# Performance work log

Measured on AMD Instinct MI355X. Metric: run time of the kernel, lower is better.

The kernel has to match this reference:

```python
import jax, jax.numpy as jnp
import numpy as np

NEG = -1e30  # log-space 'zero' (avoids -inf NaN issues under jit)
EPS = 1e-7   # keras.backend.epsilon()


def _ctc_loss(y_true, y_pred):
    # y_true: [B, L] int labels in [0, C-1), y_pred: [B, T, C] softmax probs.
    # Keras ctc_batch_cost: logits = log(y_pred + eps), then tf.nn.ctc_loss
    # (which applies log_softmax internally), blank = C - 1.
    B, T, C = y_pred.shape
    L = y_true.shape[1]
    S = 2 * L + 1
    blank = C - 1

    logp = jax.nn.log_softmax(jnp.log(y_pred + EPS), axis=-1)  # [B, T, C]

    # Extended label sequence: blank, l1, blank, l2, ..., blank  -> [B, S]
    ext = jnp.full((B, S), blank, dtype=y_true.dtype).at[:, 1::2].set(y_true)
    lp_ext = jnp.take_along_axis(logp, ext[:, None, :].astype(jnp.int32), axis=2)  # [B, T, S]

    # skip transition s-2 -> s allowed iff ext[s] != blank and ext[s] != ext[s-2]
    ext_m2 = jnp.concatenate([jnp.full((B, 2), blank, ext.dtype), ext[:, :-2]], axis=1)
    allow_skip = (ext != blank) & (ext != ext_m2)
    allow_skip = allow_skip.at[:, :2].set(False)

    # alpha init at t=0
    alpha = jnp.full((B, S), NEG, dtype=logp.dtype)
    alpha = alpha.at[:, 0].set(lp_ext[:, 0, 0]).at[:, 1].set(lp_ext[:, 0, 1])

    neg1 = jnp.full((B, 1), NEG, dtype=logp.dtype)
    neg2 = jnp.full((B, 2), NEG, dtype=logp.dtype)

    def step(a, lp_t):
        prev1 = jnp.concatenate([neg1, a[:, :-1]], axis=1)
        prev2 = jnp.concatenate([neg2, a[:, :-2]], axis=1)
        acc = jnp.logaddexp(a, prev1)
        acc = jnp.where(allow_skip, jnp.logaddexp(acc, prev2), acc)
        return acc + lp_t, None

    lp_seq = jnp.transpose(lp_ext, (1, 0, 2))[1:]  # [T-1, B, S]
    alpha, _ = jax.lax.scan(step, alpha, lp_seq)

    loss = -jnp.logaddexp(alpha[:, -1], alpha[:, -2])  # [B]
    return loss[:, None]  # [B, 1] like keras ctc_batch_cost


def setup_inputs() -> dict:
    key = jax.random.key(0)
    k1, k2 = jax.random.split(key)
    B, T, C, L = 1024, 256, 128, 64
    y_true = jax.random.randint(k1, (B, L), 0, C - 1, dtype=jnp.int32)
    y_pred = jax.random.uniform(k2, (B, T, C), dtype=jnp.float32, minval=1e-4, maxval=1.0)
    return {"y_true": y_true, "y_pred": y_pred}


def reference(y_true, y_pred):
    return _ctc_loss(y_true, y_pred)
```

## Files before the change

kernel.cpp:

```cpp
#include <hip/hip_runtime.h>
#include <math.h>

#define BATCH 1024
#define TT    256
#define CC    128
#define LL    64
#define EPSV  (1e-7f)

typedef float f32x4 __attribute__((ext_vector_type(4)));

template <int CTRL>
__device__ __forceinline__ float dpp0(float x) {
    return __int_as_float(__builtin_amdgcn_update_dpp(0, __float_as_int(x), CTRL, 0xF, 0xF, true));
}
template <int CTRL>
__device__ __forceinline__ float dppS(float x) {
    return __int_as_float(__builtin_amdgcn_update_dpp(__float_as_int(x), __float_as_int(x), CTRL, 0xF, 0xF, false));
}
__device__ __forceinline__ float rol1_f(float x) {
    return __int_as_float(__builtin_amdgcn_update_dpp(__float_as_int(x), __float_as_int(x), 0x134, 0xF, 0xF, false));
}
__device__ __forceinline__ int rol1_i(int x) {
    return __builtin_amdgcn_update_dpp(x, x, 0x134, 0xF, 0xF, false);
}
__device__ __forceinline__ float rdlane(float x, int l) {
    return __int_as_float(__builtin_amdgcn_readlane(__float_as_int(x), l));
}
__device__ __forceinline__ float wave_max_bcast(float m) {
    m = fmaxf(m, dppS<0x111>(m));
    m = fmaxf(m, dppS<0x112>(m));
    m = fmaxf(m, dppS<0x114>(m));
    m = fmaxf(m, dppS<0x118>(m));
    m = fmaxf(m, dppS<0x142>(m));
    m = fmaxf(m, dppS<0x143>(m));
    return rdlane(m, 63);
}
__device__ __forceinline__ unsigned f2h(float x) {
    _Float16 h = (_Float16)x;
    unsigned short u; __builtin_memcpy(&u, &h, 2);
    return (unsigned)u;
}
__device__ __forceinline__ float h2f(unsigned short u) {
    _Float16 h; __builtin_memcpy(&h, &u, 2);
    return (float)h;
}

__global__ __launch_bounds__(512, 8) void ctc_fwd_kernel(const int* __restrict__ y_true,
                                                         const float* __restrict__ y_pred,
                                                         float* __restrict__ out) {
    __shared__ unsigned short qtab[TT][66];
    __shared__ float qblank[TT];
    __shared__ float logZpart[8];

    const int b    = blockIdx.x;
    const int tid  = threadIdx.x;
    const int wv   = tid >> 6;
    const int lane = tid & 63;

    const float* yp = y_pred + (size_t)b * (TT * CC);
    const int lab  = y_true[b * LL + lane];
    const int srcA = lab >> 2;
    const int srcB = 32 + srcA;
    const bool hiPair = (lab & 2) != 0;
    const bool hiHalf = (lab & 1) != 0;

    const int off = ((lane >> 5) << 7) + ((lane & 31) << 2);
    const float* base = yp + off;

    float zacc = 0.0f;
    f32x4 v[4];
    #pragma unroll
    for (int j = 0; j < 4; ++j)
        v[j] = __builtin_nontemporal_load((const f32x4*)(base + 256 * (wv + 8 * j)));

    for (int g = 0; g < 4; ++g) {
        f32x4 vn[4];
        if (g < 3) {
            #pragma unroll
            for (int j = 0; j < 4; ++j)
                vn[j] = __builtin_nontemporal_load((const f32x4*)(base + 256 * (wv + 32 * (g + 1) + 8 * j)));
        }
        #pragma unroll
        for (int j = 0; j < 4; ++j) {
            const int r2 = wv + 32 * g + 8 * j;
            const int tA = 2 * r2, tB = tA + 1;
            float q0 = v[j][0] + EPSV, q1 = v[j][1] + EPSV;
            float q2 = v[j][2] + EPSV, q3 = v[j][3] + EPSV;
            float s = (q0 + q1) + (q2 + q3);
            s += dpp0<0x111>(s);
            s += dpp0<0x112>(s);
            s += dpp0<0x114>(s);
            s += dpp0<0x118>(s);
            s += dpp0<0x142>(s);
            zacc += __logf(s);
            int i01 = (int)(f2h(q0) | (f2h(q1) << 16));
            int i23 = (int)(f2h(q2) | (f2h(q3) << 16));
            int gA01 = __shfl(i01, srcA), gA23 = __shfl(i23, srcA);
            int gB01 = __shfl(i01, srcB), gB23 = __shfl(i23, srcB);
            int sA = hiPair ? gA23 : gA01;
            int sB = hiPair ? gB23 : gB01;
            qtab[tA][lane] = (unsigned short)(hiHalf ? ((unsigned)sA >> 16) : (sA & 0xFFFF));
            qtab[tB][lane] = (unsigned short)(hiHalf ? ((unsigned)sB >> 16) : (sB & 0xFFFF));
            if ((lane & 31) == 31) qblank[tA + (lane >> 5)] = q3;
        }
        #pragma unroll
        for (int j = 0; j < 4; ++j) v[j] = vn[j];
    }
    {
        float z31 = rdlane(zacc, 31), z63 = rdlane(zacc, 63);
        if (lane == 0) logZpart[wv] = z31 + z63;
    }
    __syncthreads();

    if (wv == 0) {
        float logZ = 0.0f;
        #pragma unroll
        for (int w = 0; w < 8; ++w) logZ += logZpart[w];

        const int labm1  = rol1_i(lab);
        const float mskip = (lane >= 1 && lab != labm1) ? 1.0f : 0.0f;
        const bool l0 = (lane == 0);

        float a0 = l0 ? qblank[0] : 0.0f;
        float a1 = l0 ? h2f(qtab[0][lane]) : 0.0f;
        float aX = 0.0f;
        int Esum = 0;

        float qbv[8], qlv[8];
        #pragma unroll
        for (int i = 0; i < 8; ++i) {
            qbv[i] = qblank[1 + i];
            qlv[i] = h2f(qtab[1 + i][lane]);
        }

        for (int t0 = 1; t0 + 8 <= TT; t0 += 8) {
            float qbn[8], qln[8];
            #pragma unroll
            for (int i = 0; i < 8; ++i) {
                int tn = t0 + 8 + i; tn = (tn < TT) ? tn : (TT - 1);
                qbn[i] = qblank[tn];
                qln[i] = h2f(qtab[tn][lane]);
            }
            #pragma unroll
            for (int i = 0; i < 8; ++i) {
                float nb  = rol1_f(a1);
                float na0 = (a0 + (l0 ? 0.0f : nb)) * qbv[i];
                float na1 = fmaf(mskip, nb, a0 + a1) * qlv[i];
                aX = l0 ? (aX + nb) * qbv[i] : 0.0f;
                a0 = na0; a1 = na1;
            }
            float m = fmaxf(fmaxf(a0, a1), aX);
            float mall = wave_max_bcast(m);
            int ex = (int)((__float_as_uint(mall) >> 23) & 0xFF);
            int e  = 127 - ex;
            float sc = __uint_as_float((unsigned)(127 + e) << 23);
            a0 *= sc; a1 *= sc; aX *= sc;
            Esum += e;
            #pragma unroll
            for (int i = 0; i < 8; ++i) { qbv[i] = qbn[i]; qlv[i] = qln[i]; }
        }
        #pragma unroll
        for (int i = 0; i < 7; ++i) {
            float nb  = rol1_f(a1);
            float na0 = (a0 + (l0 ? 0.0f : nb)) * qbv[i];
            float na1 = fmaf(mskip, nb, a0 + a1) * qlv[i];
            aX = l0 ? (aX + nb) * qbv[i] : 0.0f;
            a0 = na0; a1 = na1;
        }
        float a127 = rdlane(a1, 63);
        if (lane == 0) {
            float tot = aX + a127;
            out[b] = logZ + (float)Esum * 0.69314718055994531f - __logf(tot);
        }
    }
}

extern "C" void kernel_launch(void* const* d_in, const int* in_sizes, int n_in,
                              void* d_out, int out_size, void* d_ws, size_t ws_size,
                              hipStream_t stream) {
    const int*   y_true = (const int*)d_in[0];
    const float* y_pred = (const float*)d_in[1];
    float*       out    = (float*)d_out;
    ctc_fwd_kernel<<<BATCH, 512, 0, stream>>>(y_true, y_pred, out);
}
```

Before: 37.38 us.

## Interleave CTC alpha recursion with staged probability loading per time chunk

Splits the time axis into four stages with a block barrier after each. Wave 0 runs the alpha recursion on the finished chunk while the other waves load and convert the next chunk, so the serial scan no longer waits for the whole table to be built. Loads switch from nontemporal to ordinary, and the next chunk's prefetch now comes after the current chunk is processed. The trade-off is three extra barriers, raised priority for wave 0, and possible stalls when the scan stage takes longer than the load stage.

```diff
diff --git a/kernel.cpp b/kernel.cpp
--- a/kernel.cpp
+++ b/kernel.cpp
@@ -67,19 +67,20 @@
     const int off = ((lane >> 5) << 7) + ((lane & 31) << 2);
     const float* base = yp + off;
 
+    const int   labm1 = rol1_i(lab);
+    const float mskip = (lane >= 1 && lab != labm1) ? 1.0f : 0.0f;
+    const bool  l0 = (lane == 0);
+    float a0 = 0.0f, a1 = 0.0f, aX = 0.0f;
+    int   Esum = 0;
     float zacc = 0.0f;
+
     f32x4 v[4];
     #pragma unroll
     for (int j = 0; j < 4; ++j)
-        v[j] = __builtin_nontemporal_load((const f32x4*)(base + 256 * (wv + 8 * j)));
+        v[j] = *(const f32x4*)(base + 256 * (wv + 8 * j));
 
+    #pragma unroll
     for (int g = 0; g < 4; ++g) {
-        f32x4 vn[4];
-        if (g < 3) {
-            #pragma unroll
-            for (int j = 0; j < 4; ++j)
-                vn[j] = __builtin_nontemporal_load((const f32x4*)(base + 256 * (wv + 32 * (g + 1) + 8 * j)));
-        }
         #pragma unroll
         for (int j = 0; j < 4; ++j) {
             const int r2 = wv + 32 * g + 8 * j;
@@ -103,74 +104,74 @@
             qtab[tB][lane] = (unsigned short)(hiHalf ? ((unsigned)sB >> 16) : (sB & 0xFFFF));
             if ((lane & 31) == 31) qblank[tA + (lane >> 5)] = q3;
         }
-        #pragma unroll
-        for (int j = 0; j < 4; ++j) v[j] = vn[j];
+        if (g < 3) {
+            #pragma unroll
+            for (int j = 0; j < 4; ++j)
+                v[j] = *(const f32x4*)(base + 256 * (wv + 32 * (g + 1) + 8 * j));
+        }
+        if (g == 3) {
+            float z31 = rdlane(zacc, 31), z63 = rdlane(zacc, 63);
+            if (lane == 0) logZpart[wv] = z31 + z63;
+        }
+        asm volatile("s_waitcnt lgkmcnt(0)" ::: "memory");
+        __builtin_amdgcn_s_barrier();
+        __builtin_amdgcn_sched_barrier(0);
+
+        if (wv == 0) {
+            __builtin_amdgcn_s_setprio(1);
+            if (g == 0) {
+                a0 = l0 ? qblank[0] : 0.0f;
+                a1 = l0 ? h2f(qtab[0][lane]) : 0.0f;
+                aX = 0.0f;
+            }
+            const int s0 = (g == 0) ? 1 : (64 * g - 7);
+            const int nc = (g == 0) ? 7 : 8;
+            for (int c = 0; c < nc; ++c) {
+                const int s = s0 + 8 * c;
+                float qb[8], ql[8];
+                #pragma unroll
+                for (int i = 0; i < 8; ++i) {
+                    qb[i] = qblank[s + i];
+                    ql[i] = h2f(qtab[s + i][lane]);
+                }
+                #pragma unroll
+                for (int i = 0; i < 8; ++i) {
+                    float nb  = rol1_f(a1);
+                    float na0 = (a0 + (l0 ? 0.0f : nb)) * qb[i];
+                    float na1 = fmaf(mskip, nb, a0 + a1) * ql[i];
+                    aX = l0 ? (aX + nb) * qb[i] : 0.0f;
+                    a0 = na0; a1 = na1;
+                }
+                float m = fmaxf(fmaxf(a0, a1), aX);
+                float mall = wave_max_bcast(m);
+                int ex = (int)((__float_as_uint(mall) >> 23) & 0xFF);
+                int e  = 127 - ex;
+                float sc = __uint_as_float((unsigned)(127 + e) << 23);
+                a0 *= sc; a1 *= sc; aX *= sc;
+                Esum += e;
+            }
+            __builtin_amdgcn_s_setprio(0);
+        }
     }
-    {
-        float z31 = rdlane(zacc, 31), z63 = rdlane(zacc, 63);
-        if (lane == 0) logZpart[wv] = z31 + z63;
-    }
-    __syncthreads();
 
     if (wv == 0) {
-        float logZ = 0.0f;
-        #pragma unroll
-        for (int w = 0; w < 8; ++w) logZ += logZpart[w];
-
-        const int labm1  = rol1_i(lab);
-        const float mskip = (lane >= 1 && lab != labm1) ? 1.0f : 0.0f;
-        const bool l0 = (lane == 0);
-
-        float a0 = l0 ? qblank[0] : 0.0f;
-        float a1 = l0 ? h2f(qtab[0][lane]) : 0.0f;
-        float aX = 0.0f;
-        int Esum = 0;
-
-        float qbv[8], qlv[8];
-        #pragma unroll
-        for (int i = 0; i < 8; ++i) {
-            qbv[i] = qblank[1 + i];
-            qlv[i] = h2f(qtab[1 + i][lane]);
-        }
-
-        for (int t0 = 1; t0 + 8 <= TT; t0 += 8) {
-            float qbn[8], qln[8];
-            #pragma unroll
-            for (int i = 0; i < 8; ++i) {
-                int tn = t0 + 8 + i; tn = (tn < TT) ? tn : (TT - 1);
-                qbn[i] = qblank[tn];
-                qln[i] = h2f(qtab[tn][lane]);
-            }
-            #pragma unroll
-            for (int i = 0; i < 8; ++i) {
-                float nb  = rol1_f(a1);
-                float na0 = (a0 + (l0 ? 0.0f : nb)) * qbv[i];
-                float na1 = fmaf(mskip, nb, a0 + a1) * qlv[i];
-                aX = l0 ? (aX + nb) * qbv[i] : 0.0f;
-                a0 = na0; a1 = na1;
-            }
-            float m = fmaxf(fmaxf(a0, a1), aX);
-            float mall = wave_max_bcast(m);
-            int ex = (int)((__float_as_uint(mall) >> 23) & 0xFF);
-            int e  = 127 - ex;
-            float sc = __uint_as_float((unsigned)(127 + e) << 23);
-            a0 *= sc; a1 *= sc; aX *= sc;
-            Esum += e;
-            #pragma unroll
-            for (int i = 0; i < 8; ++i) { qbv[i] = qbn[i]; qlv[i] = qln[i]; }
-        }
         #pragma unroll
         for (int i = 0; i < 7; ++i) {
+            float qb = qblank[249 + i];
+            float ql = h2f(qtab[249 + i][lane]);
             float nb  = rol1_f(a1);
-            float na0 = (a0 + (l0 ? 0.0f : nb)) * qbv[i];
-            float na1 = fmaf(mskip, nb, a0 + a1) * qlv[i];
-            aX = l0 ? (aX + nb) * qbv[i] : 0.0f;
+            float na0 = (a0 + (l0 ? 0.0f : nb)) * qb;
+            float na1 = fmaf(mskip, nb, a0 + a1) * ql;
+            aX = l0 ? (aX + nb) * qb : 0.0f;
             a0 = na0; a1 = na1;
         }
+        float LZ = 0.0f;
+        #pragma unroll
+        for (int w = 0; w < 8; ++w) LZ += logZpart[w];
         float a127 = rdlane(a1, 63);
         if (lane == 0) {
             float tot = aX + a127;
-            out[b] = logZ + (float)Esum * 0.69314718055994531f - __logf(tot);
+            out[b] = LZ + (float)Esum * 0.69314718055994531f - __logf(tot);
         }
     }
 }
```

Result: slower. 46.22 us (+23.6%).

## Process four batch items per block, overlapping the DP with the next item's loads

Applied to the files above, without the earlier changes.

Each block now handles four batch items with double-buffered shared tables. Wave 0 runs the serial alpha recursion for the current item at raised priority, while the other seven waves stream and pack the next item's probabilities. This hides the single-wave DP latency behind memory traffic. In exchange there are four times fewer blocks (256), more shared memory per block, plain loads in place of nontemporal ones, and the first item is not overlapped.

```diff
diff --git a/kernel.cpp b/kernel.cpp
--- a/kernel.cpp
+++ b/kernel.cpp
@@ -6,6 +6,8 @@
 #define CC    128
 #define LL    64
 #define EPSV  (1e-7f)
+#define ITEMS 4
+#define NBLK  (BATCH / ITEMS)
 
 typedef float f32x4 __attribute__((ext_vector_type(4)));
 
@@ -45,133 +47,157 @@
     return (float)h;
 }
 
-__global__ __launch_bounds__(512, 8) void ctc_fwd_kernel(const int* __restrict__ y_true,
-                                                         const float* __restrict__ y_pred,
-                                                         float* __restrict__ out) {
-    __shared__ unsigned short qtab[TT][66];
-    __shared__ float qblank[TT];
-    __shared__ float logZpart[8];
-
-    const int b    = blockIdx.x;
-    const int tid  = threadIdx.x;
-    const int wv   = tid >> 6;
-    const int lane = tid & 63;
-
-    const float* yp = y_pred + (size_t)b * (TT * CC);
-    const int lab  = y_true[b * LL + lane];
-    const int srcA = lab >> 2;
-    const int srcB = 32 + srcA;
+template <int NPAIRS, int STRIDE, int DEPTH>
+__device__ __forceinline__ void stream_item(const float* __restrict__ base,
+                                            int start, int lab, int lane,
+                                            unsigned short (* __restrict__ qt)[66],
+                                            float* __restrict__ qb,
+                                            float* __restrict__ lzslot) {
+    const int  srcA   = lab >> 2;
+    const int  srcB   = 32 + srcA;
     const bool hiPair = (lab & 2) != 0;
     const bool hiHalf = (lab & 1) != 0;
 
-    const int off = ((lane >> 5) << 7) + ((lane & 31) << 2);
-    const float* base = yp + off;
-
     float zacc = 0.0f;
-    f32x4 v[4];
-    #pragma unroll
-    for (int j = 0; j < 4; ++j)
-        v[j] = __builtin_nontemporal_load((const f32x4*)(base + 256 * (wv + 8 * j)));
-
-    for (int g = 0; g < 4; ++g) {
-        f32x4 vn[4];
-        if (g < 3) {
-            #pragma unroll
-            for (int j = 0; j < 4; ++j)
-                vn[j] = __builtin_nontemporal_load((const f32x4*)(base + 256 * (wv + 32 * (g + 1) + 8 * j)));
-        }
-        #pragma unroll
-        for (int j = 0; j < 4; ++j) {
-            const int r2 = wv + 32 * g + 8 * j;
-            const int tA = 2 * r2, tB = tA + 1;
-            float q0 = v[j][0] + EPSV, q1 = v[j][1] + EPSV;
-            float q2 = v[j][2] + EPSV, q3 = v[j][3] + EPSV;
-            float s = (q0 + q1) + (q2 + q3);
-            s += dpp0<0x111>(s);
-            s += dpp0<0x112>(s);
-            s += dpp0<0x114>(s);
-            s += dpp0<0x118>(s);
-            s += dpp0<0x142>(s);
-            zacc += __logf(s);
-            int i01 = (int)(f2h(q0) | (f2h(q1) << 16));
-            int i23 = (int)(f2h(q2) | (f2h(q3) << 16));
-            int gA01 = __shfl(i01, srcA), gA23 = __shfl(i23, srcA);
-            int gB01 = __shfl(i01, srcB), gB23 = __shfl(i23, srcB);
-            int sA = hiPair ? gA23 : gA01;
-            int sB = hiPair ? gB23 : gB01;
-            qtab[tA][lane] = (unsigned short)(hiHalf ? ((unsigned)sA >> 16) : (sA & 0xFFFF));
-            qtab[tB][lane] = (unsigned short)(hiHalf ? ((unsigned)sB >> 16) : (sB & 0xFFFF));
-            if ((lane & 31) == 31) qblank[tA + (lane >> 5)] = q3;
-        }
-        #pragma unroll
-        for (int j = 0; j < 4; ++j) v[j] = vn[j];
-    }
-    {
-        float z31 = rdlane(zacc, 31), z63 = rdlane(zacc, 63);
-        if (lane == 0) logZpart[wv] = z31 + z63;
-    }
-    __syncthreads();
-
-    if (wv == 0) {
-        float logZ = 0.0f;
-        #pragma unroll
-        for (int w = 0; w < 8; ++w) logZ += logZpart[w];
-
-        const int labm1  = rol1_i(lab);
-        const float mskip = (lane >= 1 && lab != labm1) ? 1.0f : 0.0f;
-        const bool l0 = (lane == 0);
-
-        float a0 = l0 ? qblank[0] : 0.0f;
-        float a1 = l0 ? h2f(qtab[0][lane]) : 0.0f;
-        float aX = 0.0f;
-        int Esum = 0;
-
-        float qbv[8], qlv[8];
+    f32x4 v[DEPTH];
+    #pragma unroll
+    for (int d = 0; d < DEPTH; ++d) {
+        int r2 = start + STRIDE * d; r2 = (r2 < 128) ? r2 : 127;
+        v[d] = *(const f32x4*)(base + 256 * r2);
+    }
+    #pragma unroll
+    for (int i = 0; i < NPAIRS; ++i) {
+        const int  r2i   = start + STRIDE * i;
+        const bool valid = (r2i < 128);
+        const int  r2    = valid ? r2i : 127;
+        f32x4 x = v[i % DEPTH];
+        if (i + DEPTH < NPAIRS) {
+            int rn = start + STRIDE * (i + DEPTH); rn = (rn < 128) ? rn : 127;
+            v[i % DEPTH] = *(const f32x4*)(base + 256 * rn);
+        }
+        const int tA = 2 * r2, tB = tA + 1;
+        float q0 = x[0] + EPSV, q1 = x[1] + EPSV;
+        float q2 = x[2] + EPSV, q3 = x[3] + EPSV;
+        float s = (q0 + q1) + (q2 + q3);
+        s += dpp0<0x111>(s);
+        s += dpp0<0x112>(s);
+        s += dpp0<0x114>(s);
+        s += dpp0<0x118>(s);
+        s += dpp0<0x142>(s);
+        if (valid) zacc += __logf(s);
+        int i01 = (int)(f2h(q0) | (f2h(q1) << 16));
+        int i23 = (int)(f2h(q2) | (f2h(q3) << 16));
+        int gA01 = __shfl(i01, srcA), gA23 = __shfl(i23, srcA);
+        int gB01 = __shfl(i01, srcB), gB23 = __shfl(i23, srcB);
+        int sA = hiPair ? gA23 : gA01;
+        int sB = hiPair ? gB23 : gB01;
+        qt[tA][lane] = (unsigned short)(hiHalf ? ((unsigned)sA >> 16) : (sA & 0xFFFF));
+        qt[tB][lane] = (unsigned short)(hiHalf ? ((unsigned)sB >> 16) : (sB & 0xFFFF));
+        if ((lane & 31) == 31) qb[tA + (lane >> 5)] = q3;
+    }
+    float z31 = rdlane(zacc, 31), z63 = rdlane(zacc, 63);
+    if (lane == 0) *lzslot = z31 + z63;
+}
+
+__device__ __forceinline__ void run_dp(int bglob, int lane,
+                                       const int* __restrict__ y_true,
+                                       const unsigned short (* __restrict__ qt)[66],
+                                       const float* __restrict__ qb_,
+                                       const float* __restrict__ lz, int lzFirst,
+                                       float* __restrict__ out) {
+    const int   lab   = y_true[bglob * LL + lane];
+    const int   labm1 = rol1_i(lab);
+    const float mskip = (lane >= 1 && lab != labm1) ? 1.0f : 0.0f;
+    const bool  l0 = (lane == 0);
+
+    float a0 = l0 ? qb_[0] : 0.0f;
+    float a1 = l0 ? h2f(qt[0][lane]) : 0.0f;
+    float aX = 0.0f;
+    int Esum = 0;
+
+    float qbv[8], qlv[8];
+    #pragma unroll
+    for (int i = 0; i < 8; ++i) {
+        qbv[i] = qb_[1 + i];
+        qlv[i] = h2f(qt[1 + i][lane]);
+    }
+    for (int t0 = 1; t0 + 8 <= TT; t0 += 8) {
+        float qbn[8], qln[8];
         #pragma unroll
         for (int i = 0; i < 8; ++i) {
-            qbv[i] = qblank[1 + i];
-            qlv[i] = h2f(qtab[1 + i][lane]);
-        }
-
-        for (int t0 = 1; t0 + 8 <= TT; t0 += 8) {
-            float qbn[8], qln[8];
-            #pragma unroll
-            for (int i = 0; i < 8; ++i) {
-                int tn = t0 + 8 + i; tn = (tn < TT) ? tn : (TT - 1);
-                qbn[i] = qblank[tn];
-                qln[i] = h2f(qtab[tn][lane]);
-            }
-            #pragma unroll
-            for (int i = 0; i < 8; ++i) {
-                float nb  = rol1_f(a1);
-                float na0 = (a0 + (l0 ? 0.0f : nb)) * qbv[i];
-                float na1 = fmaf(mskip, nb, a0 + a1) * qlv[i];
-                aX = l0 ? (aX + nb) * qbv[i] : 0.0f;
-                a0 = na0; a1 = na1;
-            }
-            float m = fmaxf(fmaxf(a0, a1), aX);
-            float mall = wave_max_bcast(m);
-            int ex = (int)((__float_as_uint(mall) >> 23) & 0xFF);
-            int e  = 127 - ex;
-            float sc = __uint_as_float((unsigned)(127 + e) << 23);
-            a0 *= sc; a1 *= sc; aX *= sc;
-            Esum += e;
-            #pragma unroll
-            for (int i = 0; i < 8; ++i) { qbv[i] = qbn[i]; qlv[i] = qln[i]; }
+            int tn = t0 + 8 + i; tn = (tn < TT) ? tn : (TT - 1);
+            qbn[i] = qb_[tn];
+            qln[i] = h2f(qt[tn][lane]);
         }
         #pragma unroll
-        for (int i = 0; i < 7; ++i) {
+        for (int i = 0; i < 8; ++i) {
             float nb  = rol1_f(a1);
             float na0 = (a0 + (l0 ? 0.0f : nb)) * qbv[i];
             float na1 = fmaf(mskip, nb, a0 + a1) * qlv[i];
             aX = l0 ? (aX + nb) * qbv[i] : 0.0f;
             a0 = na0; a1 = na1;
         }
-        float a127 = rdlane(a1, 63);
-        if (lane == 0) {
-            float tot = aX + a127;
-            out[b] = logZ + (float)Esum * 0.69314718055994531f - __logf(tot);
-        }
+        float m = fmaxf(fmaxf(a0, a1), aX);
+        float mall = wave_max_bcast(m);
+        int ex = (int)((__float_as_uint(mall) >> 23) & 0xFF);
+        int e  = 127 - ex;
+        float sc = __uint_as_float((unsigned)(127 + e) << 23);
+        a0 *= sc; a1 *= sc; aX *= sc;
+        Esum += e;
+        #pragma unroll
+        for (int i = 0; i < 8; ++i) { qbv[i] = qbn[i]; qlv[i] = qln[i]; }
+    }
+    #pragma unroll
+    for (int i = 0; i < 7; ++i) {
+        float nb  = rol1_f(a1);
+        float na0 = (a0 + (l0 ? 0.0f : nb)) * qbv[i];
+        float na1 = fmaf(mskip, nb, a0 + a1) * qlv[i];
+        aX = l0 ? (aX + nb) * qbv[i] : 0.0f;
+        a0 = na0; a1 = na1;
+    }
+    float LZ = 0.0f;
+    for (int w = lzFirst; w < 8; ++w) LZ += lz[w];
+    float a127 = rdlane(a1, 63);
+    if (lane == 0) {
+        out[bglob] = LZ + (float)Esum * 0.69314718055994531f - __logf(aX + a127);
+    }
+}
+
+__global__ __launch_bounds__(512, 2) void ctc_fwd_kernel(const int* __restrict__ y_true,
+                                                         const float* __restrict__ y_pred,
+                                                         float* __restrict__ out) {
+    __shared__ unsigned short qtab[2][TT][66];
+    __shared__ float qblank[2][TT];
+    __shared__ float logZpart[2][8];
+
+    const int tid  = threadIdx.x;
+    const int wv   = tid >> 6;
+    const int lane = tid & 63;
+    const int b0   = blockIdx.x * ITEMS;
+    const int off  = ((lane >> 5) << 7) + ((lane & 31) << 2);
+
+    {
+        int lab = y_true[b0 * LL + lane];
+        stream_item<16, 8, 6>(y_pred + (size_t)b0 * (TT * CC) + off, wv, lab, lane,
+                              qtab[0], qblank[0], &logZpart[0][wv]);
+    }
+    __syncthreads();
+
+    for (int i = 0; i < ITEMS; ++i) {
+        const int cur = i & 1;
+        if (wv > 0 && i + 1 < ITEMS) {
+            const int bnx = b0 + i + 1;
+            int lab = y_true[bnx * LL + lane];
+            stream_item<19, 7, 6>(y_pred + (size_t)bnx * (TT * CC) + off, wv - 1, lab, lane,
+                                  qtab[cur ^ 1], qblank[cur ^ 1], &logZpart[cur ^ 1][wv]);
+        }
+        if (wv == 0) {
+            __builtin_amdgcn_s_setprio(1);
+            run_dp(b0 + i, lane, y_true, qtab[cur], qblank[cur],
+                   logZpart[cur], (i == 0) ? 0 : 1, out);
+            __builtin_amdgcn_s_setprio(0);
+        }
+        if (i + 1 < ITEMS) __syncthreads();
     }
 }
 
@@ -181,5 +207,5 @@
     const int*   y_true = (const int*)d_in[0];
     const float* y_pred = (const float*)d_in[1];
     float*       out    = (float*)d_out;
-    ctc_fwd_kernel<<<BATCH, 512, 0, stream>>>(y_true, y_pred, out);
-}
+    ctc_fwd_kernel<<<NBLK, 512, 0, stream>>>(y_true, y_pred, out);
+}
```

Measured after the change: 60.66 us. 62.3% more time.

## Split CTC into staging kernel and separate single-wave DP kernel via workspace

Applied to the files above, without the earlier changes.

Splits the fused kernel into two launches. The first writes the gathered fp16 label probabilities, the blank probabilities and partial log-normalisers to a global workspace. The second runs the alpha recursion with one 64-thread wave per batch element, double-buffering chunk loads from global memory. The aim is to stop the serial DP from leaving seven waves of a 512-thread block idle, and to let many small DP blocks share each CU. The cost is an extra launch plus roughly 34 MB of workspace written and read back through global memory.

```diff
diff --git a/kernel.cpp b/kernel.cpp
--- a/kernel.cpp
+++ b/kernel.cpp
@@ -6,6 +6,13 @@
 #define CC    128
 #define LL    64
 #define EPSV  (1e-7f)
+
+#define QT_BYTES  ((size_t)BATCH * TT * 64 * 2)
+#define QB_OFF    QT_BYTES
+#define QB_BYTES  ((size_t)BATCH * TT * 4)
+#define LZ_OFF    (QB_OFF + QB_BYTES)
+#define LZ_BYTES  ((size_t)BATCH * 8 * 4)
+#define WS_NEEDED (LZ_OFF + LZ_BYTES)
 
 typedef float f32x4 __attribute__((ext_vector_type(4)));
 
@@ -43,6 +50,147 @@
 __device__ __forceinline__ float h2f(unsigned short u) {
     _Float16 h; __builtin_memcpy(&h, &u, 2);
     return (float)h;
+}
+
+__global__ __launch_bounds__(512, 8) void ctc_stage_kernel(const int* __restrict__ y_true,
+                                                           const float* __restrict__ y_pred,
+                                                           unsigned short* __restrict__ qt_g,
+                                                           float* __restrict__ qb_g,
+                                                           float* __restrict__ lz_g) {
+    const int b    = blockIdx.x;
+    const int tid  = threadIdx.x;
+    const int wv   = tid >> 6;
+    const int lane = tid & 63;
+
+    const float* yp = y_pred + (size_t)b * (TT * CC);
+    const int lab  = y_true[b * LL + lane];
+    const int srcA = lab >> 2;
+    const int srcB = 32 + srcA;
+    const bool hiPair = (lab & 2) != 0;
+    const bool hiHalf = (lab & 1) != 0;
+
+    const int off = ((lane >> 5) << 7) + ((lane & 31) << 2);
+    const float* base = yp + off;
+    unsigned short* qt = qt_g + (size_t)b * (TT * 64);
+    float* qb = qb_g + b * TT;
+
+    float zacc = 0.0f;
+    f32x4 v[6];
+    #pragma unroll
+    for (int d = 0; d < 6; ++d)
+        v[d] = __builtin_nontemporal_load((const f32x4*)(base + 256 * (wv + 8 * d)));
+
+    #pragma unroll
+    for (int i = 0; i < 16; ++i) {
+        f32x4 x = v[i % 6];
+        if (i + 6 < 16)
+            v[i % 6] = __builtin_nontemporal_load((const f32x4*)(base + 256 * (wv + 8 * (i + 6))));
+        const int r2 = wv + 8 * i;
+        const int tA = 2 * r2, tB = tA + 1;
+        float q0 = x[0] + EPSV, q1 = x[1] + EPSV;
+        float q2 = x[2] + EPSV, q3 = x[3] + EPSV;
+        float s = (q0 + q1) + (q2 + q3);
+        s += dpp0<0x111>(s);
+        s += dpp0<0x112>(s);
+        s += dpp0<0x114>(s);
+        s += dpp0<0x118>(s);
+        s += dpp0<0x142>(s);
+        zacc += __logf(s);
+        int i01 = (int)(f2h(q0) | (f2h(q1) << 16));
+        int i23 = (int)(f2h(q2) | (f2h(q3) << 16));
+        int gA01 = __shfl(i01, srcA), gA23 = __shfl(i23, srcA);
+        int gB01 = __shfl(i01, srcB), gB23 = __shfl(i23, srcB);
+        int sA = hiPair ? gA23 : gA01;
+        int sB = hiPair ? gB23 : gB01;
+        qt[tA * 64 + lane] = (unsigned short)(hiHalf ? ((unsigned)sA >> 16) : (sA & 0xFFFF));
+        qt[tB * 64 + lane] = (unsigned short)(hiHalf ? ((unsigned)sB >> 16) : (sB & 0xFFFF));
+        if ((lane & 31) == 31) qb[tA + (lane >> 5)] = q3;
+    }
+    float z31 = rdlane(zacc, 31), z63 = rdlane(zacc, 63);
+    if (lane == 0) lz_g[b * 8 + wv] = z31 + z63;
+}
+
+__device__ __forceinline__ void load_chunk8(const unsigned short* __restrict__ qt,
+                                            const float* __restrict__ qb,
+                                            int lane, int t0,
+                                            float (&qbo)[8], float (&qlo)[8]) {
+    #pragma unroll
+    for (int i = 0; i < 8; ++i) {
+        int t = t0 + i; t = (t < TT) ? t : (TT - 1);
+        qbo[i] = qb[t];
+        qlo[i] = h2f(qt[t * 64 + lane]);
+    }
+}
+__device__ __forceinline__ void steps8(const float (&qbv)[8], const float (&qlv)[8],
+                                       float& a0, float& a1, float& aX,
+                                       float mskip, bool l0, int& Esum) {
+    #pragma unroll
+    for (int i = 0; i < 8; ++i) {
+        float nb  = rol1_f(a1);
+        float na0 = (a0 + (l0 ? 0.0f : nb)) * qbv[i];
+        float na1 = fmaf(mskip, nb, a0 + a1) * qlv[i];
+        aX = l0 ? (aX + nb) * qbv[i] : 0.0f;
+        a0 = na0; a1 = na1;
+    }
+    float m = fmaxf(fmaxf(a0, a1), aX);
+    float mall = wave_max_bcast(m);
+    int ex = (int)((__float_as_uint(mall) >> 23) & 0xFF);
+    int e  = 127 - ex;
+    float sc = __uint_as_float((unsigned)(127 + e) << 23);
+    a0 *= sc; a1 *= sc; aX *= sc;
+    Esum += e;
+}
+
+__global__ __launch_bounds__(64, 4) void ctc_dp_kernel(const int* __restrict__ y_true,
+                                                       const unsigned short* __restrict__ qt_g,
+                                                       const float* __restrict__ qb_g,
+                                                       const float* __restrict__ lz_g,
+                                                       float* __restrict__ out) {
+    const int b    = blockIdx.x;
+    const int lane = threadIdx.x;
+    const unsigned short* qt = qt_g + (size_t)b * (TT * 64);
+    const float* qb = qb_g + b * TT;
+
+    const int   lab   = y_true[b * LL + lane];
+    const int   labm1 = rol1_i(lab);
+    const float mskip = (lane >= 1 && lab != labm1) ? 1.0f : 0.0f;
+    const bool  l0 = (lane == 0);
+
+    float a0 = l0 ? qb[0] : 0.0f;
+    float a1 = l0 ? h2f(qt[lane]) : 0.0f;
+    float aX = 0.0f;
+    int Esum = 0;
+
+    float qbA[8], qlA[8], qbB[8], qlB[8], qbC[8], qlC[8], qbD[8], qlD[8];
+    load_chunk8(qt, qb, lane, 1, qbA, qlA);
+    load_chunk8(qt, qb, lane, 9, qbB, qlB);
+
+    for (int it = 0; it < 15; ++it) {
+        load_chunk8(qt, qb, lane, 17 + 16 * it, qbC, qlC);
+        steps8(qbA, qlA, a0, a1, aX, mskip, l0, Esum);
+        load_chunk8(qt, qb, lane, 25 + 16 * it, qbD, qlD);
+        steps8(qbB, qlB, a0, a1, aX, mskip, l0, Esum);
+        #pragma unroll
+        for (int i = 0; i < 8; ++i) {
+            qbA[i] = qbC[i]; qlA[i] = qlC[i];
+            qbB[i] = qbD[i]; qlB[i] = qlD[i];
+        }
+    }
+    steps8(qbA, qlA, a0, a1, aX, mskip, l0, Esum);
+    #pragma unroll
+    for (int i = 0; i < 7; ++i) {
+        float nb  = rol1_f(a1);
+        float na0 = (a0 + (l0 ? 0.0f : nb)) * qbB[i];
+        float na1 = fmaf(mskip, nb, a0 + a1) * qlB[i];
+        aX = l0 ? (aX + nb) * qbB[i] : 0.0f;
+        a0 = na0; a1 = na1;
+    }
+    float LZ = 0.0f;
+    #pragma unroll
+    for (int w = 0; w < 8; ++w) LZ += lz_g[b * 8 + w];
+    float a127 = rdlane(a1, 63);
+    if (lane == 0)
+        out[b] = LZ + (float)Esum * 0.69314718055994531f - __logf(aX + a127);
 }
 
 __global__ __launch_bounds__(512, 8) void ctc_fwd_kernel(const int* __restrict__ y_true,
@@ -116,8 +264,7 @@
         float logZ = 0.0f;
         #pragma unroll
         for (int w = 0; w < 8; ++w) logZ += logZpart[w];
-
-        const int labm1  = rol1_i(lab);
+        const int labm1 = rol1_i(lab);
         const float mskip = (lane >= 1 && lab != labm1) ? 1.0f : 0.0f;
         const bool l0 = (lane == 0);
 
@@ -132,7 +279,6 @@
             qbv[i] = qblank[1 + i];
             qlv[i] = h2f(qtab[1 + i][lane]);
         }
-
         for (int t0 = 1; t0 + 8 <= TT; t0 += 8) {
             float qbn[8], qln[8];
             #pragma unroll
@@ -169,8 +315,7 @@
         }
         float a127 = rdlane(a1, 63);
         if (lane == 0) {
-            float tot = aX + a127;
-            out[b] = logZ + (float)Esum * 0.69314718055994531f - __logf(tot);
+            out[b] = logZ + (float)Esum * 0.69314718055994531f - __logf(aX + a127);
         }
     }
 }
@@ -181,5 +326,13 @@
     const int*   y_true = (const int*)d_in[0];
     const float* y_pred = (const float*)d_in[1];
     float*       out    = (float*)d_out;
-    ctc_fwd_kernel<<<BATCH, 512, 0, stream>>>(y_true, y_pred, out);
-}
+    if (ws_size >= WS_NEEDED) {
+        unsigned short* qt_g = (unsigned short*)d_ws;
+        float* qb_g = (float*)((char*)d_ws + QB_OFF);
+        float* lz_g = (float*)((char*)d_ws + LZ_OFF);
+        ctc_stage_kernel<<<BATCH, 512, 0, stream>>>(y_true, y_pred, qt_g, qb_g, lz_g);
+        ctc_dp_kernel<<<BATCH, 64, 0, stream>>>(y_true, qt_g, qb_g, lz_g, out);
+    } else {
+        ctc_fwd_kernel<<<BATCH, 512, 0, stream>>>(y_true, y_pred, out);
+    }
+}
```

New measurement: 49.10 us. 1.31x slower.
